# Kernel optimization log

Hardware: AMD Instinct MI355X
Metric: run time of the kernel (lower is better)

## Reference

```python
import jax, jax.numpy as jnp
import numpy as np

HEAD_DIM = 64

def setup_inputs() -> dict:
    key = jax.random.key(0)
    k1, k2, k3, k4 = jax.random.split(key, 4)
    B, S, D, H = 8, 2048, 1024, HEAD_DIM
    x = jax.random.normal(k1, (B, S, D), dtype=jnp.float32)
    scale = 1.0 / np.sqrt(D)
    W_q = jax.random.normal(k2, (H, D), dtype=jnp.float32) * scale
    W_k = jax.random.normal(k3, (H, D), dtype=jnp.float32) * scale
    W_v = jax.random.normal(k4, (H, D), dtype=jnp.float32) * scale
    return {"input_embeddings": x, "W_q": W_q, "W_k": W_k, "W_v": W_v}

def reference(input_embeddings, W_q, W_k, W_v):
    # Linear(model_dim, head_dim, bias=False): y = x @ W.T
    q = jnp.einsum('bsd,hd->bsh', input_embeddings, W_q)
    k = jnp.einsum('bsd,hd->bsh', input_embeddings, W_k)
    v = jnp.einsum('bsd,hd->bsh', input_embeddings, W_v)
    scores = jnp.einsum('bqh,bkh->bqk', q, k) / jnp.sqrt(jnp.float32(HEAD_DIM))
    S = scores.shape[-1]
    causal = jnp.tril(jnp.ones((S, S), dtype=bool))  # [S,S]
    scores = jnp.where(causal, scores, -jnp.inf)
    attn = jax.nn.softmax(scores, axis=-1)
    # dropout p=0.0 (eval-equivalent): identity
    return jnp.einsum('bqk,bkh->bqh', attn, v)
```

## Files before the change

### kernel.cpp

```cpp
#include <hip/hip_runtime.h>
#include <hip/hip_bf16.h>

typedef __bf16 bf16x8 __attribute__((ext_vector_type(8)));
typedef __bf16 bf16x4 __attribute__((ext_vector_type(4)));
typedef float  f32x4  __attribute__((ext_vector_type(4)));

#define NB  8
#define SEQ 2048
#define DM  1024
#define HD  64

#define WAITV5 asm volatile("s_waitcnt vmcnt(5)" ::: "memory")
#define WAITV0 asm volatile("s_waitcnt vmcnt(0)" ::: "memory")

__device__ __forceinline__ void gll16(const void* g, void* l) {
    __builtin_amdgcn_global_load_lds(
        (const __attribute__((address_space(1))) unsigned int*)g,
        (__attribute__((address_space(3))) unsigned int*)l, 16, 0, 0);
}

__global__ void k_convw(const float* __restrict__ Wq, const float* __restrict__ Wk,
                        const float* __restrict__ Wv, __bf16* __restrict__ Wb) {
    int idx = blockIdx.x * blockDim.x + threadIdx.x;
    int e = idx * 4;
    const float* src;
    if (e < 65536)       src = Wq + e;
    else if (e < 131072) src = Wk + (e - 65536);
    else                 src = Wv + (e - 131072);
    float4 v = *reinterpret_cast<const float4*>(src);
    bf16x4 o;
    o[0] = (__bf16)v.x; o[1] = (__bf16)v.y; o[2] = (__bf16)v.z; o[3] = (__bf16)v.w;
    *reinterpret_cast<bf16x4*>(Wb + e) = o;
}

__launch_bounds__(512)
__global__ void k_proj(const float* __restrict__ X, const __bf16* __restrict__ Wb,
                       __bf16* __restrict__ Qb, __bf16* __restrict__ Kb,
                       __bf16* __restrict__ Vt) {
    __shared__ __align__(16) float  Xs[3][4096];
    __shared__ __align__(16) __bf16 Ws[3][12288];
    const int tid = threadIdx.x;
    const int w = tid >> 6, l = tid & 63;
    const int lr = l & 15, lg = l >> 4;
    const int wm = w >> 2, wn = w & 3;
    const int m0 = blockIdx.x * 64;

    const float* xsrc[2];
    #pragma unroll
    for (int j = 0; j < 2; ++j) {
        int ux = w * 128 + j * 64 + l;
        int r_ = ux >> 4, c_ = ux & 15;
        xsrc[j] = X + (size_t)(m0 + r_) * DM + (c_ ^ (r_ & 15)) * 4;
    }
    const __bf16* wsrc[3];
    #pragma unroll
    for (int j = 0; j < 3; ++j) {
        int uw = w * 192 + j * 64 + l;
        int r_ = uw >> 3, c_ = uw & 7;
        wsrc[j] = Wb + (size_t)r_ * DM + (c_ ^ (r_ & 7)) * 8;
    }

    f32x4 acc[2][3];
    #pragma unroll
    for (int mt = 0; mt < 2; ++mt)
        #pragma unroll
        for (int ct = 0; ct < 3; ++ct)
            acc[mt][ct] = f32x4{0.f, 0.f, 0.f, 0.f};

    int abase[2], bbase[3];
    #pragma unroll
    for (int mt = 0; mt < 2; ++mt) abase[mt] = (wm * 32 + mt * 16 + lr) * 64;
    #pragma unroll
    for (int ct = 0; ct < 3; ++ct) bbase[ct] = ((wn * 3 + ct) * 16 + lr) * 64;

    #pragma unroll
    for (int t = 0; t < 2; ++t) {
        #pragma unroll
        for (int j = 0; j < 2; ++j) gll16(xsrc[j] + t * 64, &Xs[t][w * 512 + j * 256]);
        #pragma unroll
        for (int j = 0; j < 3; ++j) gll16(wsrc[j] + t * 64, &Ws[t][w * 1536 + j * 512]);
    }

    int sl = 0;
    for (int t = 0; t < 16; ++t) {
        if (t < 15) WAITV5; else WAITV0;
        __builtin_amdgcn_s_barrier();
        if (t + 2 < 16) {
            int si = sl + 2; if (si >= 3) si -= 3;
            #pragma unroll
            for (int j = 0; j < 2; ++j)
                gll16(xsrc[j] + (t + 2) * 64, &Xs[si][w * 512 + j * 256]);
            #pragma unroll
            for (int j = 0; j < 3; ++j)
                gll16(wsrc[j] + (t + 2) * 64, &Ws[si][w * 1536 + j * 512]);
        }
        const float*  Xp = &Xs[sl][0];
        const __bf16* Wp = &Ws[sl][0];
        #pragma unroll
        for (int ks = 0; ks < 2; ++ks) {
            bf16x8 af[2];
            #pragma unroll
            for (int mt = 0; mt < 2; ++mt) {
                f32x4 a0 = *reinterpret_cast<const f32x4*>(Xp + abase[mt] + ((ks * 8 + lg * 2)     ^ lr) * 4);
                f32x4 a1 = *reinterpret_cast<const f32x4*>(Xp + abase[mt] + ((ks * 8 + lg * 2 + 1) ^ lr) * 4);
                #pragma unroll
                for (int j = 0; j < 4; ++j) { af[mt][j] = (__bf16)a0[j]; af[mt][4 + j] = (__bf16)a1[j]; }
            }
            #pragma unroll
            for (int ct = 0; ct < 3; ++ct) {
                bf16x8 bf = *reinterpret_cast<const bf16x8*>(
                    Wp + bbase[ct] + (((ks * 4 + lg) ^ (lr & 7)) * 8));
                #pragma unroll
                for (int mt = 0; mt < 2; ++mt)
                    acc[mt][ct] = __builtin_amdgcn_mfma_f32_16x16x32_bf16(af[mt], bf, acc[mt][ct], 0, 0, 0);
            }
        }
        ++sl; if (sl >= 3) sl = 0;
    }

    #pragma unroll
    for (int mt = 0; mt < 2; ++mt) {
        const int rowbase = m0 + wm * 32 + mt * 16 + lg * 4;
        #pragma unroll
        for (int ct = 0; ct < 3; ++ct) {
            const int ntile = wn * 3 + ct;
            const int mtx = ntile >> 2;
            const int d = (ntile & 3) * 16 + lr;
            if (mtx == 0) {
                #pragma unroll
                for (int r = 0; r < 4; ++r)
                    Qb[(size_t)(rowbase + r) * HD + d] = (__bf16)(acc[mt][ct][r] * 0.125f);
            } else if (mtx == 1) {
                #pragma unroll
                for (int r = 0; r < 4; ++r)
                    Kb[(size_t)(rowbase + r) * HD + d] = (__bf16)acc[mt][ct][r];
            } else {
                int bb = rowbase >> 11;
                int s0 = rowbase & 2047;
                bf16x4 vv;
                #pragma unroll
                for (int r = 0; r < 4; ++r) vv[r] = (__bf16)acc[mt][ct][r];
                *reinterpret_cast<bf16x4*>(Vt + ((size_t)bb * HD + d) * SEQ + s0) = vv;
            }
        }
    }
}

__launch_bounds__(256)
__global__ void k_attn(const __bf16* __restrict__ Qb, const __bf16* __restrict__ Kb,
                       const __bf16* __restrict__ Vt, __bf16* __restrict__ Opart,
                       float* __restrict__ ML, int T, int NC) {
    const int bid = blockIdx.x;
    const int b = bid / (32 * NC);
    const int rem = bid - b * 32 * NC;
    const int qt = rem / NC;
    const int c = rem - qt * NC;
    if (c * T > qt) return;
    const int kt0 = c * T;
    const int nt = min(T, qt + 1 - kt0);
    const int q0 = qt * 64;

    __shared__ __align__(16) __bf16 Ks[64][72];
    __shared__ __align__(16) __bf16 Vs[64][72];
    __shared__ __align__(16) __bf16 Ps[64][72];
    const int tid = threadIdx.x;
    const int w = tid >> 6, l = tid & 63;
    const int lr = l & 15, lg = l >> 4;
    const __bf16* Qp = Qb + (size_t)b * SEQ * HD;
    const __bf16* Kp = Kb + (size_t)b * SEQ * HD;
    const __bf16* Vp = Vt + (size_t)b * HD * SEQ;

    const int srow = tid >> 3, sc8 = (tid & 7) * 8;
    const int myq = q0 + 16 * w + lr;

    bf16x8 qa[2];
    #pragma unroll
    for (int ks = 0; ks < 2; ++ks)
        qa[ks] = *reinterpret_cast<const bf16x8*>(
            Qp + (size_t)(q0 + 16 * w + lr) * HD + ks * 32 + lg * 8);

    bf16x8 kpre[2], vpre[2];
    {
        const int k0 = kt0 * 64;
        #pragma unroll
        for (int i = 0; i < 2; ++i) {
            int row = srow + 32 * i;
            kpre[i] = *reinterpret_cast<const bf16x8*>(Kp + (size_t)(k0 + row) * HD + sc8);
            vpre[i] = *reinterpret_cast<const bf16x8*>(Vp + (size_t)row * SEQ + k0 + sc8);
        }
    }

    f32x4 oacc[4];
    #pragma unroll
    for (int r = 0; r < 4; ++r) oacc[r] = f32x4{0.f, 0.f, 0.f, 0.f};
    float m = -1e30f, lsum = 0.f;

    for (int it = 0; it < nt; ++it) {
        const int kt = kt0 + it;
        const int k0 = kt * 64;
        __syncthreads();
        #pragma unroll
        for (int i = 0; i < 2; ++i) {
            int row = srow + 32 * i;
            *reinterpret_cast<bf16x8*>(&Ks[row][sc8]) = kpre[i];
            *reinterpret_cast<bf16x8*>(&Vs[row][sc8]) = vpre[i];
        }
        __syncthreads();
        if (it + 1 < nt) {
            const int k0n = (kt + 1) * 64;
            #pragma unroll
            for (int i = 0; i < 2; ++i) {
                int row = srow + 32 * i;
                kpre[i] = *reinterpret_cast<const bf16x8*>(Kp + (size_t)(k0n + row) * HD + sc8);
                vpre[i] = *reinterpret_cast<const bf16x8*>(Vp + (size_t)row * SEQ + k0n + sc8);
            }
        }

        f32x4 sacc[4];
        #pragma unroll
        for (int t = 0; t < 4; ++t) sacc[t] = f32x4{0.f, 0.f, 0.f, 0.f};
        #pragma unroll
        for (int ks = 0; ks < 2; ++ks) {
            #pragma unroll
            for (int t = 0; t < 4; ++t) {
                bf16x8 kf = *reinterpret_cast<const bf16x8*>(&Ks[16 * t + lr][ks * 32 + lg * 8]);
                sacc[t] = __builtin_amdgcn_mfma_f32_16x16x32_bf16(kf, qa[ks], sacc[t], 0, 0, 0);
            }
        }

        const bool diag = (kt == qt);
        float pmax = -1e30f;
        #pragma unroll
        for (int t = 0; t < 4; ++t)
            #pragma unroll
            for (int r = 0; r < 4; ++r) {
                float v = sacc[t][r];
                if (diag && (k0 + 16 * t + lg * 4 + r) > myq) v = -1e30f;
                sacc[t][r] = v;
                pmax = fmaxf(pmax, v);
            }
        pmax = fmaxf(pmax, __shfl_xor(pmax, 16));
        pmax = fmaxf(pmax, __shfl_xor(pmax, 32));
        float mnew = fmaxf(m, pmax);
        float fsc = __expf(m - mnew);
        m = mnew;
        float rs = 0.f;
        #pragma unroll
        for (int t = 0; t < 4; ++t)
            #pragma unroll
            for (int r = 0; r < 4; ++r) {
                float p = __expf(sacc[t][r] - mnew);
                sacc[t][r] = p;
                rs += p;
            }
        rs += __shfl_xor(rs, 16);
        rs += __shfl_xor(rs, 32);
        lsum = lsum * fsc + rs;

        #pragma unroll
        for (int r = 0; r < 4; ++r) {
            float fq = __shfl(fsc, (l & 48) + lg * 4 + r);
            #pragma unroll
            for (int t2 = 0; t2 < 4; ++t2) oacc[t2][r] *= fq;
        }

        #pragma unroll
        for (int t = 0; t < 4; ++t) {
            bf16x4 pv;
            #pragma unroll
            for (int r = 0; r < 4; ++r) pv[r] = (__bf16)sacc[t][r];
            *reinterpret_cast<bf16x4*>(&Ps[16 * w + lr][16 * t + lg * 4]) = pv;
        }

        #pragma unroll
        for (int ks = 0; ks < 2; ++ks) {
            bf16x8 pa = *reinterpret_cast<const bf16x8*>(&Ps[16 * w + lr][ks * 32 + lg * 8]);
            #pragma unroll
            for (int t2 = 0; t2 < 4; ++t2) {
                bf16x8 vb = *reinterpret_cast<const bf16x8*>(&Vs[16 * t2 + lr][ks * 32 + lg * 8]);
                oacc[t2] = __builtin_amdgcn_mfma_f32_16x16x32_bf16(pa, vb, oacc[t2], 0, 0, 0);
            }
        }
    }

    const size_t slot = (size_t)bid;
    __bf16* op = Opart + slot * 4096;
    #pragma unroll
    for (int t2 = 0; t2 < 4; ++t2)
        #pragma unroll
        for (int r = 0; r < 4; ++r)
            op[(16 * w + lg * 4 + r) * 64 + 16 * t2 + lr] = (__bf16)oacc[t2][r];
    if (lg == 0) {
        float* ml = ML + slot * 128;
        int row = 16 * w + lr;
        ml[row * 2]     = m;
        ml[row * 2 + 1] = lsum;
    }
}

__launch_bounds__(256)
__global__ void k_merge(const __bf16* __restrict__ Opart, const float* __restrict__ ML,
                        float* __restrict__ Out, int T, int NC) {
    const int bq = blockIdx.x;
    const int qt = bq & 31;
    const int nc = qt / T + 1;
    const int row = threadIdx.x >> 2;
    const int cg = (threadIdx.x & 3) * 16;
    const int base = bq * NC;

    float M = -1e30f;
    for (int c = 0; c < nc; ++c)
        M = fmaxf(M, ML[(size_t)(base + c) * 128 + row * 2]);

    float L = 0.f;
    f32x4 a0{0,0,0,0}, a1{0,0,0,0}, a2{0,0,0,0}, a3{0,0,0,0};
    for (int c = 0; c < nc; ++c) {
        const float* ml = ML + (size_t)(base + c) * 128 + row * 2;
        float wgt = __expf(ml[0] - M);
        L += ml[1] * wgt;
        const __bf16* op = Opart + (size_t)(base + c) * 4096 + row * 64 + cg;
        bf16x8 v0 = *reinterpret_cast<const bf16x8*>(op);
        bf16x8 v1 = *reinterpret_cast<const bf16x8*>(op + 8);
        #pragma unroll
        for (int j = 0; j < 4; ++j) {
            a0[j] += wgt * (float)v0[j];
            a1[j] += wgt * (float)v0[4 + j];
            a2[j] += wgt * (float)v1[j];
            a3[j] += wgt * (float)v1[4 + j];
        }
    }
    float inv = 1.f / L;
    #pragma unroll
    for (int j = 0; j < 4; ++j) { a0[j] *= inv; a1[j] *= inv; a2[j] *= inv; a3[j] *= inv; }
    float* o = Out + ((size_t)bq * 64 + row) * 64 + cg;
    *reinterpret_cast<f32x4*>(o)      = a0;
    *reinterpret_cast<f32x4*>(o + 4)  = a1;
    *reinterpret_cast<f32x4*>(o + 8)  = a2;
    *reinterpret_cast<f32x4*>(o + 12) = a3;
}

extern "C" void kernel_launch(void* const* d_in, const int* in_sizes, int n_in,
                              void* d_out, int out_size, void* d_ws, size_t ws_size,
                              hipStream_t stream) {
    const float* x  = (const float*)d_in[0];
    const float* wq = (const float*)d_in[1];
    const float* wk = (const float*)d_in[2];
    const float* wv = (const float*)d_in[3];
    char* ws = (char*)d_ws;
    __bf16* Wb = (__bf16*)ws;
    __bf16* Qb = (__bf16*)(ws + 524288);
    __bf16* Kb = (__bf16*)(ws + 524288 + 2097152);
    __bf16* Vt = (__bf16*)(ws + 524288 + 2 * 2097152);
    const size_t base = 524288 + 3 * 2097152;
    float* out = (float*)d_out;

    int T;
    if (ws_size >= base + (size_t)2048 * 8704)      T = 4;
    else if (ws_size >= base + (size_t)1024 * 8704) T = 8;
    else                                            T = 32;
    const int NC = 32 / T;
    const int slots = 8 * 32 * NC;
    float*  ML    = (float*)(ws + base);
    __bf16* Opart = (__bf16*)(ws + base + (size_t)slots * 512);

    hipLaunchKernelGGL(k_convw, dim3(192), dim3(256), 0, stream, wq, wk, wv, Wb);
    hipLaunchKernelGGL(k_proj,  dim3(256), dim3(512), 0, stream, x, Wb, Qb, Kb, Vt);
    hipLaunchKernelGGL(k_attn,  dim3(8 * 32 * NC), dim3(256), 0, stream,
                       Qb, Kb, Vt, Opart, ML, T, NC);
    hipLaunchKernelGGL(k_merge, dim3(256), dim3(256), 0, stream, Opart, ML, out, T, NC);
}
```

Before: 60.76 us.

## Use 128-row query tiles, exp2 softmax with lazy rescale, skip masked waves

New measurement: 59.76 us. No clear change (-1.6%).

```diff
diff --git a/kernel.cpp b/kernel.cpp
--- a/kernel.cpp
+++ b/kernel.cpp
@@ -129,7 +129,7 @@
             if (mtx == 0) {
                 #pragma unroll
                 for (int r = 0; r < 4; ++r)
-                    Qb[(size_t)(rowbase + r) * HD + d] = (__bf16)(acc[mt][ct][r] * 0.125f);
+                    Qb[(size_t)(rowbase + r) * HD + d] = (__bf16)(acc[mt][ct][r] * 0.18033688f);
             } else if (mtx == 1) {
                 #pragma unroll
                 for (int r = 0; r < 4; ++r)
@@ -146,23 +146,24 @@
     }
 }
 
-__launch_bounds__(256)
+__launch_bounds__(512)
 __global__ void k_attn(const __bf16* __restrict__ Qb, const __bf16* __restrict__ Kb,
                        const __bf16* __restrict__ Vt, __bf16* __restrict__ Opart,
                        float* __restrict__ ML, int T, int NC) {
     const int bid = blockIdx.x;
-    const int b = bid / (32 * NC);
-    const int rem = bid - b * 32 * NC;
-    const int qt = rem / NC;
-    const int c = rem - qt * NC;
-    if (c * T > qt) return;
+    const int b = bid / (16 * NC);
+    const int rem = bid - b * 16 * NC;
+    const int qt2 = rem / NC;
+    const int c = rem - qt2 * NC;
+    const int kmax = 2 * qt2 + 1;
+    if (c * T > kmax) return;
     const int kt0 = c * T;
-    const int nt = min(T, qt + 1 - kt0);
-    const int q0 = qt * 64;
+    const int nt = min(T, kmax + 1 - kt0);
+    const int q0 = qt2 * 128;
 
     __shared__ __align__(16) __bf16 Ks[64][72];
     __shared__ __align__(16) __bf16 Vs[64][72];
-    __shared__ __align__(16) __bf16 Ps[64][72];
+    __shared__ __align__(16) __bf16 Ps[128][72];
     const int tid = threadIdx.x;
     const int w = tid >> 6, l = tid & 63;
     const int lr = l & 15, lg = l >> 4;
@@ -177,17 +178,13 @@
     #pragma unroll
     for (int ks = 0; ks < 2; ++ks)
         qa[ks] = *reinterpret_cast<const bf16x8*>(
-            Qp + (size_t)(q0 + 16 * w + lr) * HD + ks * 32 + lg * 8);
-
-    bf16x8 kpre[2], vpre[2];
+            Qp + (size_t)myq * HD + ks * 32 + lg * 8);
+
+    bf16x8 kpre, vpre;
     {
         const int k0 = kt0 * 64;
-        #pragma unroll
-        for (int i = 0; i < 2; ++i) {
-            int row = srow + 32 * i;
-            kpre[i] = *reinterpret_cast<const bf16x8*>(Kp + (size_t)(k0 + row) * HD + sc8);
-            vpre[i] = *reinterpret_cast<const bf16x8*>(Vp + (size_t)row * SEQ + k0 + sc8);
-        }
+        kpre = *reinterpret_cast<const bf16x8*>(Kp + (size_t)(k0 + srow) * HD + sc8);
+        vpre = *reinterpret_cast<const bf16x8*>(Vp + (size_t)srow * SEQ + k0 + sc8);
     }
 
     f32x4 oacc[4];
@@ -199,22 +196,16 @@
         const int kt = kt0 + it;
         const int k0 = kt * 64;
         __syncthreads();
-        #pragma unroll
-        for (int i = 0; i < 2; ++i) {
-            int row = srow + 32 * i;
-            *reinterpret_cast<bf16x8*>(&Ks[row][sc8]) = kpre[i];
-            *reinterpret_cast<bf16x8*>(&Vs[row][sc8]) = vpre[i];
-        }
+        *reinterpret_cast<bf16x8*>(&Ks[srow][sc8]) = kpre;
+        *reinterpret_cast<bf16x8*>(&Vs[srow][sc8]) = vpre;
         __syncthreads();
         if (it + 1 < nt) {
-            const int k0n = (kt + 1) * 64;
-            #pragma unroll
-            for (int i = 0; i < 2; ++i) {
-                int row = srow + 32 * i;
-                kpre[i] = *reinterpret_cast<const bf16x8*>(Kp + (size_t)(k0n + row) * HD + sc8);
-                vpre[i] = *reinterpret_cast<const bf16x8*>(Vp + (size_t)row * SEQ + k0n + sc8);
-            }
-        }
+            const int k0n = k0 + 64;
+            kpre = *reinterpret_cast<const bf16x8*>(Kp + (size_t)(k0n + srow) * HD + sc8);
+            vpre = *reinterpret_cast<const bf16x8*>(Vp + (size_t)srow * SEQ + k0n + sc8);
+        }
+
+        if (k0 > q0 + 16 * w + 15) continue;
 
         f32x4 sacc[4];
         #pragma unroll
@@ -228,41 +219,51 @@
             }
         }
 
-        const bool diag = (kt == qt);
         float pmax = -1e30f;
-        #pragma unroll
-        for (int t = 0; t < 4; ++t)
-            #pragma unroll
-            for (int r = 0; r < 4; ++r) {
-                float v = sacc[t][r];
-                if (diag && (k0 + 16 * t + lg * 4 + r) > myq) v = -1e30f;
-                sacc[t][r] = v;
-                pmax = fmaxf(pmax, v);
-            }
+        if (k0 + 63 > q0 + 16 * w) {
+            #pragma unroll
+            for (int t = 0; t < 4; ++t)
+                #pragma unroll
+                for (int r = 0; r < 4; ++r) {
+                    float v = sacc[t][r];
+                    if ((k0 + 16 * t + lg * 4 + r) > myq) v = -1e30f;
+                    sacc[t][r] = v;
+                    pmax = fmaxf(pmax, v);
+                }
+        } else {
+            #pragma unroll
+            for (int t = 0; t < 4; ++t)
+                #pragma unroll
+                for (int r = 0; r < 4; ++r) pmax = fmaxf(pmax, sacc[t][r]);
+        }
         pmax = fmaxf(pmax, __shfl_xor(pmax, 16));
         pmax = fmaxf(pmax, __shfl_xor(pmax, 32));
-        float mnew = fmaxf(m, pmax);
-        float fsc = __expf(m - mnew);
-        m = mnew;
+
+        if (!__all(pmax <= m + 12.f)) {
+            float mnew = fmaxf(m, pmax);
+            float fsc = exp2f(m - mnew);
+            m = mnew;
+            lsum *= fsc;
+            #pragma unroll
+            for (int r = 0; r < 4; ++r) {
+                float fq = __shfl(fsc, (l & 48) + lg * 4 + r);
+                #pragma unroll
+                for (int t2 = 0; t2 < 4; ++t2) oacc[t2][r] *= fq;
+            }
+        }
+
         float rs = 0.f;
         #pragma unroll
         for (int t = 0; t < 4; ++t)
             #pragma unroll
             for (int r = 0; r < 4; ++r) {
-                float p = __expf(sacc[t][r] - mnew);
+                float p = exp2f(sacc[t][r] - m);
                 sacc[t][r] = p;
                 rs += p;
             }
         rs += __shfl_xor(rs, 16);
         rs += __shfl_xor(rs, 32);
-        lsum = lsum * fsc + rs;
-
-        #pragma unroll
-        for (int r = 0; r < 4; ++r) {
-            float fq = __shfl(fsc, (l & 48) + lg * 4 + r);
-            #pragma unroll
-            for (int t2 = 0; t2 < 4; ++t2) oacc[t2][r] *= fq;
-        }
+        lsum += rs;
 
         #pragma unroll
         for (int t = 0; t < 4; ++t) {
@@ -284,59 +285,56 @@
     }
 
     const size_t slot = (size_t)bid;
-    __bf16* op = Opart + slot * 4096;
+    __bf16* op = Opart + slot * 8192;
     #pragma unroll
     for (int t2 = 0; t2 < 4; ++t2)
         #pragma unroll
         for (int r = 0; r < 4; ++r)
             op[(16 * w + lg * 4 + r) * 64 + 16 * t2 + lr] = (__bf16)oacc[t2][r];
     if (lg == 0) {
-        float* ml = ML + slot * 128;
+        float* ml = ML + slot * 256;
         int row = 16 * w + lr;
         ml[row * 2]     = m;
         ml[row * 2 + 1] = lsum;
     }
 }
 
-__launch_bounds__(256)
+__launch_bounds__(512)
 __global__ void k_merge(const __bf16* __restrict__ Opart, const float* __restrict__ ML,
                         float* __restrict__ Out, int T, int NC) {
-    const int bq = blockIdx.x;
-    const int qt = bq & 31;
-    const int nc = qt / T + 1;
-    const int row = threadIdx.x >> 2;
-    const int cg = (threadIdx.x & 3) * 16;
-    const int base = bq * NC;
+    const int bq2 = blockIdx.x >> 1;
+    const int half = blockIdx.x & 1;
+    const int qt2 = bq2 & 15;
+    const int nc = (2 * qt2 + 1) / T + 1;
+    const int tid = threadIdx.x;
+    const int row = tid >> 2;
+    const int cg = (tid & 3) * 8 + half * 32;
+    const int base = bq2 * NC;
 
     float M = -1e30f;
     for (int c = 0; c < nc; ++c)
-        M = fmaxf(M, ML[(size_t)(base + c) * 128 + row * 2]);
+        M = fmaxf(M, ML[(size_t)(base + c) * 256 + row * 2]);
 
     float L = 0.f;
-    f32x4 a0{0,0,0,0}, a1{0,0,0,0}, a2{0,0,0,0}, a3{0,0,0,0};
+    f32x4 a0{0,0,0,0}, a1{0,0,0,0};
     for (int c = 0; c < nc; ++c) {
-        const float* ml = ML + (size_t)(base + c) * 128 + row * 2;
-        float wgt = __expf(ml[0] - M);
+        const float* ml = ML + (size_t)(base + c) * 256 + row * 2;
+        float wgt = exp2f(ml[0] - M);
         L += ml[1] * wgt;
-        const __bf16* op = Opart + (size_t)(base + c) * 4096 + row * 64 + cg;
-        bf16x8 v0 = *reinterpret_cast<const bf16x8*>(op);
-        bf16x8 v1 = *reinterpret_cast<const bf16x8*>(op + 8);
+        bf16x8 v = *reinterpret_cast<const bf16x8*>(
+            Opart + (size_t)(base + c) * 8192 + row * 64 + cg);
         #pragma unroll
         for (int j = 0; j < 4; ++j) {
-            a0[j] += wgt * (float)v0[j];
-            a1[j] += wgt * (float)v0[4 + j];
-            a2[j] += wgt * (float)v1[j];
-            a3[j] += wgt * (float)v1[4 + j];
+            a0[j] += wgt * (float)v[j];
+            a1[j] += wgt * (float)v[4 + j];
         }
     }
     float inv = 1.f / L;
     #pragma unroll
-    for (int j = 0; j < 4; ++j) { a0[j] *= inv; a1[j] *= inv; a2[j] *= inv; a3[j] *= inv; }
-    float* o = Out + ((size_t)bq * 64 + row) * 64 + cg;
-    *reinterpret_cast<f32x4*>(o)      = a0;
-    *reinterpret_cast<f32x4*>(o + 4)  = a1;
-    *reinterpret_cast<f32x4*>(o + 8)  = a2;
-    *reinterpret_cast<f32x4*>(o + 12) = a3;
+    for (int j = 0; j < 4; ++j) { a0[j] *= inv; a1[j] *= inv; }
+    float* o = Out + ((size_t)bq2 * 128 + row) * 64 + cg;
+    *reinterpret_cast<f32x4*>(o)     = a0;
+    *reinterpret_cast<f32x4*>(o + 4) = a1;
 }
 
 extern "C" void kernel_launch(void* const* d_in, const int* in_sizes, int n_in,
@@ -354,18 +352,15 @@
     const size_t base = 524288 + 3 * 2097152;
     float* out = (float*)d_out;
 
-    int T;
-    if (ws_size >= base + (size_t)2048 * 8704)      T = 4;
-    else if (ws_size >= base + (size_t)1024 * 8704) T = 8;
-    else                                            T = 32;
-    const int NC = 32 / T;
-    const int slots = 8 * 32 * NC;
+    int NC = (ws_size >= base + (size_t)(8 * 16 * 8) * 17408) ? 8 : 2;
+    int T = 32 / NC;
+    const int slots = 8 * 16 * NC;
     float*  ML    = (float*)(ws + base);
-    __bf16* Opart = (__bf16*)(ws + base + (size_t)slots * 512);
+    __bf16* Opart = (__bf16*)(ws + base + (size_t)slots * 1024);
 
     hipLaunchKernelGGL(k_convw, dim3(192), dim3(256), 0, stream, wq, wk, wv, Wb);
     hipLaunchKernelGGL(k_proj,  dim3(256), dim3(512), 0, stream, x, Wb, Qb, Kb, Vt);
-    hipLaunchKernelGGL(k_attn,  dim3(8 * 32 * NC), dim3(256), 0, stream,
+    hipLaunchKernelGGL(k_attn,  dim3(8 * 16 * NC), dim3(512), 0, stream,
                        Qb, Kb, Vt, Opart, ML, T, NC);
-    hipLaunchKernelGGL(k_merge, dim3(256), dim3(256), 0, stream, Opart, ML, out, T, NC);
-}
+    hipLaunchKernelGGL(k_merge, dim3(256), dim3(512), 0, stream, Opart, ML, out, T, NC);
+}
```
